# Performance work log

Hardware: AMD Instinct MI355X
Metric: run time of the kernel (lower is better)

The kernel has to match this reference:

```python
import jax, jax.numpy as jnp
import numpy as np

NEG_SLOPE = 0.2


def gatv2_layer(x, src, dst, Wl, Wr, att, bias, concat):
    # PyG GATv2Conv (share_weights=False): x_l = W_l x (source), x_r = W_r x (target)
    # e_ij = att . leaky_relu(x_l[j] + x_r[i]); alpha = softmax over incoming edges at i
    N = x.shape[0]
    H, C = att.shape
    xl = (x @ Wl).reshape(N, H, C)
    xr = (x @ Wr).reshape(N, H, C)
    msg = jax.nn.leaky_relu(xl[src] + xr[dst], NEG_SLOPE)          # [E, H, C]
    logits = jnp.einsum('ehc,hc->eh', msg, att)                     # [E, H]
    mx = jax.ops.segment_max(logits, dst, num_segments=N)           # [N, H]
    ex = jnp.exp(logits - mx[dst])
    denom = jax.ops.segment_sum(ex, dst, num_segments=N)            # [N, H]
    alpha = ex / denom[dst]                                         # [E, H]
    out = jax.ops.segment_sum(alpha[:, :, None] * xl[src], dst, num_segments=N)  # [N, H, C]
    out = out.reshape(N, H * C) if concat else out.mean(axis=1)
    return out + bias


def gat_forward(x, edge_index, Wl1, Wr1, att1, b1, Wl2, Wr2, att2, b2, Wl3, Wr3, att3, b3):
    N = x.shape[0]
    loop = jnp.arange(N, dtype=edge_index.dtype)
    src = jnp.concatenate([edge_index[0], loop])  # add self loops (PyG default)
    dst = jnp.concatenate([edge_index[1], loop])
    # eval mode: feature/attention dropout are identity
    h = jax.nn.elu(gatv2_layer(x, src, dst, Wl1, Wr1, att1, b1, concat=True))
    h = jax.nn.elu(gatv2_layer(h, src, dst, Wl2, Wr2, att2, b2, concat=True))
    return gatv2_layer(h, src, dst, Wl3, Wr3, att3, b3, concat=False)


def setup_inputs() -> dict:
    key = jax.random.key(0)
    ks = jax.random.split(key, 16)
    N, E = 50000, 800000
    IN, HID, H, OUT = 256, 32, 8, 64
    D1 = HID * H  # 256
    s = 0.05
    return {
        'x': jax.random.normal(ks[0], (N, IN), dtype=jnp.float32),
        'edge_index': jax.random.randint(ks[1], (2, E), 0, N, dtype=jnp.int64),
        'Wl1': jax.random.normal(ks[2], (IN, D1), dtype=jnp.float32) * s,
        'Wr1': jax.random.normal(ks[3], (IN, D1), dtype=jnp.float32) * s,
        'att1': jax.random.normal(ks[4], (H, HID), dtype=jnp.float32) * s,
        'b1': jnp.zeros((D1,), dtype=jnp.float32),
        'Wl2': jax.random.normal(ks[5], (D1, D1), dtype=jnp.float32) * s,
        'Wr2': jax.random.normal(ks[6], (D1, D1), dtype=jnp.float32) * s,
        'att2': jax.random.normal(ks[7], (H, HID), dtype=jnp.float32) * s,
        'b2': jnp.zeros((D1,), dtype=jnp.float32),
        'Wl3': jax.random.normal(ks[8], (D1, OUT), dtype=jnp.float32) * s,
        'Wr3': jax.random.normal(ks[9], (D1, OUT), dtype=jnp.float32) * s,
        'att3': jax.random.normal(ks[10], (1, OUT), dtype=jnp.float32) * s,
        'b3': jnp.zeros((OUT,), dtype=jnp.float32),
    }


def reference(x, edge_index, Wl1, Wr1, att1, b1, Wl2, Wr2, att2, b2, Wl3, Wr3, att3, b3):
    return gat_forward(x, edge_index, Wl1, Wr1, att1, b1, Wl2, Wr2, att2, b2, Wl3, Wr3, att3, b3)
```

## Files before the change

kernel.cpp:

```cpp
#include <hip/hip_runtime.h>
#include <hip/hip_fp16.h>

#define NEG_SLOPE 0.2f

typedef __attribute__((ext_vector_type(8))) _Float16 f16x8;
typedef __attribute__((ext_vector_type(4))) float f32x4;

__device__ __forceinline__ void gload_lds16(const unsigned short* g, unsigned short* lds) {
    __builtin_amdgcn_global_load_lds(
        (const __attribute__((address_space(1))) void*)g,
        (__attribute__((address_space(3))) void*)lds, 16, 0, 0);
}

__device__ __forceinline__ void h8_to_f(const uint4 v, float* f) {
    const __half2* hp = reinterpret_cast<const __half2*>(&v);
    float2 t0 = __half22float2(hp[0]);
    float2 t1 = __half22float2(hp[1]);
    float2 t2 = __half22float2(hp[2]);
    float2 t3 = __half22float2(hp[3]);
    f[0] = t0.x; f[1] = t0.y; f[2] = t1.x; f[3] = t1.y;
    f[4] = t2.x; f[5] = t2.y; f[6] = t3.x; f[7] = t3.y;
}


__global__ void detect_i64_kernel(const unsigned int* __restrict__ w, int E, int* __restrict__ flag) {
    __shared__ unsigned int ssum[256];
    int n = E < 4096 ? E : 4096;
    unsigned int local = 0;
    for (int k = threadIdx.x; k < n; k += 256) local |= w[2 * k + 1];
    ssum[threadIdx.x] = local;
    __syncthreads();
    for (int off = 128; off > 0; off >>= 1) {
        if (threadIdx.x < off) ssum[threadIdx.x] |= ssum[threadIdx.x + off];
        __syncthreads();
    }
    if (threadIdx.x == 0) flag[0] = (ssum[0] == 0) ? 1 : 0;
}

__global__ void count_deg_kernel(const void* __restrict__ eiv, int E,
                                 const int* __restrict__ flag, int* __restrict__ deg) {
    int e = blockIdx.x * blockDim.x + threadIdx.x;
    if (e >= E) return;
    int d;
    if (*flag) d = (int)((const long long*)eiv)[(size_t)E + e];
    else       d = ((const int*)eiv)[(size_t)E + e];
    atomicAdd(&deg[d], 1);
}

__global__ void scan_block_kernel(const int* __restrict__ deg, int* __restrict__ row_ptr,
                                  int* __restrict__ partial, int N) {
    __shared__ int sd[1024];
    int t = threadIdx.x;
    int g = blockIdx.x * 1024 + t;
    int v = (g < N) ? deg[g] : 0;
    sd[t] = v;
    __syncthreads();
    for (int off = 1; off < 1024; off <<= 1) {
        int add = (t >= off) ? sd[t - off] : 0;
        __syncthreads();
        sd[t] += add;
        __syncthreads();
    }
    if (g < N) row_ptr[g + 1] = sd[t];
    if (t == 1023) partial[blockIdx.x] = sd[1023];
    if (g == 0) row_ptr[0] = 0;
}

__global__ void scan_top_kernel(int* __restrict__ partial, int nb) {
    if (threadIdx.x == 0 && blockIdx.x == 0) {
        int run = 0;
        for (int j = 0; j < nb; ++j) { run += partial[j]; partial[j] = run; }
    }
}

__global__ void scan_addoff_kernel(int* __restrict__ row_ptr, const int* __restrict__ partial, int N) {
    int g = blockIdx.x * 256 + threadIdx.x;
    if (g >= N) return;
    int b = g >> 10;
    if (b > 0) row_ptr[g + 1] += partial[b - 1];
}

__global__ void scatter_kernel(const void* __restrict__ eiv, int E,
                               const int* __restrict__ flag,
                               const int* __restrict__ row_ptr,
                               int* __restrict__ cursor, int* __restrict__ csr) {
    int e = blockIdx.x * blockDim.x + threadIdx.x;
    if (e >= E) return;
    int s, d;
    if (*flag) {
        s = (int)((const long long*)eiv)[e];
        d = (int)((const long long*)eiv)[(size_t)E + e];
    } else {
        s = ((const int*)eiv)[e];
        d = ((const int*)eiv)[(size_t)E + e];
    }
    int pos = atomicAdd(&cursor[d], 1);
    csr[row_ptr[d] + pos] = s;
}


__global__ void split_kernel(const float* __restrict__ src, int n4,
                             unsigned short* __restrict__ hi, unsigned short* __restrict__ lo) {
    int i = blockIdx.x * blockDim.x + threadIdx.x;
    if (i >= n4) return;
    float4 v = *reinterpret_cast<const float4*>(&src[(size_t)i * 4]);
    ushort4 h, l;
    __half t;
    t = __float2half(v.x); h.x = __half_as_ushort(t); l.x = __half_as_ushort(__float2half(v.x - __half2float(t)));
    t = __float2half(v.y); h.y = __half_as_ushort(t); l.y = __half_as_ushort(__float2half(v.y - __half2float(t)));
    t = __float2half(v.z); h.z = __half_as_ushort(t); l.z = __half_as_ushort(__float2half(v.z - __half2float(t)));
    t = __float2half(v.w); h.w = __half_as_ushort(t); l.w = __half_as_ushort(__float2half(v.w - __half2float(t)));
    *reinterpret_cast<ushort4*>(&hi[(size_t)i * 4]) = h;
    *reinterpret_cast<ushort4*>(&lo[(size_t)i * 4]) = l;
}

__global__ void splitT_w_kernel(const float* __restrict__ Wl, const float* __restrict__ Wr, int M,
                                unsigned short* __restrict__ WThi) {
    int k = blockIdx.x;
    int m2 = blockIdx.y * 256 + threadIdx.x;
    if (m2 >= 2 * M) return;
    float v = (m2 < M) ? Wl[(size_t)k * M + m2] : Wr[(size_t)k * M + (m2 - M)];
    WThi[(size_t)m2 * 256 + k] = __half_as_ushort(__float2half(v));
}


__global__ __launch_bounds__(256) void gemm_mfma_kernel(
    const unsigned short* __restrict__ Ahi, const unsigned short* __restrict__ Alo,
    const unsigned short* __restrict__ B,
    __half* __restrict__ xl16, float* __restrict__ xr32, int N, int M) {
    __shared__ unsigned short sA[2][128 * 64];
    __shared__ unsigned short sB[128 * 64];

    int t = threadIdx.x;
    int lane = t & 63;
    int w = t >> 6;
    int wr = (w >> 1) * 64;
    int wc = (w & 1) * 64;
    int row0 = blockIdx.x * 128;
    int n0 = blockIdx.y * 128;

    int l15 = lane & 15;
    int l4 = lane >> 4;

    int lr8 = lane >> 3;
    int lc8 = lane & 7;
    int ksw = (lc8 ^ lr8) * 8;

    f32x4 acc[4][4] = {};

    for (int k0 = 0; k0 < 256; k0 += 64) {
        __syncthreads();
        #pragma unroll
        for (int i = 0; i < 4; ++i) {
            int brow = i * 32 + w * 8;
            int row = brow + lr8;
            int ar = row0 + row; if (ar >= N) ar = N - 1;
            int bc = n0 + row;
            gload_lds16(&Ahi[(size_t)ar * 256 + k0 + ksw], &sA[0][brow * 64]);
            gload_lds16(&Alo[(size_t)ar * 256 + k0 + ksw], &sA[1][brow * 64]);
            gload_lds16(&B[(size_t)bc * 256 + k0 + ksw], &sB[brow * 64]);
        }
        __syncthreads();

        #pragma unroll
        for (int ksub = 0; ksub < 2; ++ksub) {
            int kb = ksub * 32 + l4 * 8;
            f16x8 b[4];
            #pragma unroll
            for (int fc = 0; fc < 4; ++fc) {
                int cc = wc + fc * 16 + l15;
                b[fc] = *reinterpret_cast<const f16x8*>(&sB[cc * 64 + (kb ^ ((cc & 7) << 3))]);
            }
            #pragma unroll
            for (int fr = 0; fr < 4; ++fr) {
                int r = wr + fr * 16 + l15;
                int idx = r * 64 + (kb ^ ((r & 7) << 3));
                f16x8 ah = *reinterpret_cast<const f16x8*>(&sA[0][idx]);
                f16x8 al = *reinterpret_cast<const f16x8*>(&sA[1][idx]);
                #pragma unroll
                for (int fc = 0; fc < 4; ++fc) {
                    acc[fr][fc] = __builtin_amdgcn_mfma_f32_16x16x32_f16(ah, b[fc], acc[fr][fc], 0, 0, 0);
                    acc[fr][fc] = __builtin_amdgcn_mfma_f32_16x16x32_f16(al, b[fc], acc[fr][fc], 0, 0, 0);
                }
            }
        }
    }

    #pragma unroll
    for (int fr = 0; fr < 4; ++fr) {
        #pragma unroll
        for (int j = 0; j < 4; ++j) {
            int row = row0 + wr + fr * 16 + l4 * 4 + j;
            if (row < N) {
                #pragma unroll
                for (int fc = 0; fc < 4; ++fc) {
                    int col = n0 + wc + fc * 16 + l15;
                    float v = acc[fr][fc][j];
                    if (col < M) xl16[(size_t)row * M + col] = __float2half(v);
                    else         xr32[(size_t)row * M + (col - M)] = v;
                }
            }
        }
    }
}


__global__ __launch_bounds__(256) void agg_h8_kernel(
    const __half* __restrict__ xl16, const float* __restrict__ xr32,
    const float* __restrict__ att, const float* __restrict__ bias,
    const int* __restrict__ row_ptr, const int* __restrict__ csr,
    unsigned short* __restrict__ ohi, unsigned short* __restrict__ olo, int N) {
    int wv = threadIdx.x >> 6;
    int i = blockIdx.x * 4 + wv;
    if (i >= N) return;
    int lane = threadIdx.x & 63;
    int half = lane >> 5;
    int cb = (lane & 31) * 8;

    float rxr[8], a6[8], a4[8];
    {
        float4 r0 = *reinterpret_cast<const float4*>(&xr32[(size_t)i * 256 + cb]);
        float4 r1 = *reinterpret_cast<const float4*>(&xr32[(size_t)i * 256 + cb + 4]);
        rxr[0] = r0.x; rxr[1] = r0.y; rxr[2] = r0.z; rxr[3] = r0.w;
        rxr[4] = r1.x; rxr[5] = r1.y; rxr[6] = r1.z; rxr[7] = r1.w;
        float4 w0 = *reinterpret_cast<const float4*>(&att[cb]);
        float4 w1 = *reinterpret_cast<const float4*>(&att[cb + 4]);
        float aa[8] = {w0.x, w0.y, w0.z, w0.w, w1.x, w1.y, w1.z, w1.w};
        #pragma unroll
        for (int c = 0; c < 8; ++c) { a6[c] = 0.6f * aa[c]; a4[c] = 0.4f * aa[c]; }
    }

    float acc[8], l, m;
    {
        uint4 sv = *reinterpret_cast<const uint4*>(&xl16[(size_t)i * 256 + cb]);
        float u[8];
        h8_to_f(sv, u);
        float p = 0.f;
        #pragma unroll
        for (int c = 0; c < 8; ++c) {
            float v = u[c] + rxr[c];
            p = fmaf(a6[c], v, p);
            p = fmaf(a4[c], fabsf(v), p);
        }
        p += __shfl_xor(p, 1, 4);
        p += __shfl_xor(p, 2, 4);
        m = p;
        l = half ? 0.f : 1.f;
        #pragma unroll
        for (int c = 0; c < 8; ++c) acc[c] = half ? 0.f : u[c];
    }

    int start = row_ptr[i], end = row_ptr[i + 1];

    int kk0 = start + half, kk1 = start + 2 + half;
    int s0 = (kk0 < end) ? csr[kk0] : i;
    int s1 = (kk1 < end) ? csr[kk1] : i;
    uint4 ca = *reinterpret_cast<const uint4*>(&xl16[(size_t)s0 * 256 + cb]);
    uint4 cbv = *reinterpret_cast<const uint4*>(&xl16[(size_t)s1 * 256 + cb]);

    for (int k = start; k < end; k += 4) {
        int nk0 = k + 4 + half, nk1 = k + 6 + half;
        int t0 = (nk0 < end) ? csr[nk0] : i;
        int t1 = (nk1 < end) ? csr[nk1] : i;
        uint4 na = *reinterpret_cast<const uint4*>(&xl16[(size_t)t0 * 256 + cb]);
        uint4 nb = *reinterpret_cast<const uint4*>(&xl16[(size_t)t1 * 256 + cb]);

        float ua[8], ub[8];
        h8_to_f(ca, ua);
        h8_to_f(cbv, ub);
        float p0 = 0.f, p1 = 0.f;
        #pragma unroll
        for (int c = 0; c < 8; ++c) {
            float v0 = ua[c] + rxr[c];
            p0 = fmaf(a6[c], v0, p0);
            p0 = fmaf(a4[c], fabsf(v0), p0);
            float v1 = ub[c] + rxr[c];
            p1 = fmaf(a6[c], v1, p1);
            p1 = fmaf(a4[c], fabsf(v1), p1);
        }
        p0 += __shfl_xor(p0, 1, 4);
        p0 += __shfl_xor(p0, 2, 4);
        p1 += __shfl_xor(p1, 1, 4);
        p1 += __shfl_xor(p1, 2, 4);
        float e0 = (k + half < end)     ? __expf(fminf(p0 - m, 60.f)) : 0.f;
        float e1 = (k + 2 + half < end) ? __expf(fminf(p1 - m, 60.f)) : 0.f;
        l += e0 + e1;
        #pragma unroll
        for (int c = 0; c < 8; ++c) acc[c] = fmaf(e0, ua[c], fmaf(e1, ub[c], acc[c]));

        ca = na; cbv = nb;
    }

    l += __shfl_xor(l, 32, 64);
    #pragma unroll
    for (int c = 0; c < 8; ++c) acc[c] += __shfl_xor(acc[c], 32, 64);

    if (half == 0) {
        float4 bb0 = *reinterpret_cast<const float4*>(&bias[cb]);
        float4 bb1 = *reinterpret_cast<const float4*>(&bias[cb + 4]);
        float bs[8] = {bb0.x, bb0.y, bb0.z, bb0.w, bb1.x, bb1.y, bb1.z, bb1.w};
        float inv = 1.0f / l;
        unsigned int hw[4], lw[4];
        #pragma unroll
        for (int c2 = 0; c2 < 4; ++c2) {
            float r0 = fmaf(acc[2 * c2], inv, bs[2 * c2]);
            float r1 = fmaf(acc[2 * c2 + 1], inv, bs[2 * c2 + 1]);
            r0 = (r0 > 0.f) ? r0 : (__expf(r0) - 1.f);
            r1 = (r1 > 0.f) ? r1 : (__expf(r1) - 1.f);
            __half th0 = __float2half(r0);
            __half th1 = __float2half(r1);
            unsigned short h0 = __half_as_ushort(th0), h1 = __half_as_ushort(th1);
            float f0 = r0 - __half2float(th0);
            float f1 = r1 - __half2float(th1);
            unsigned short l0 = __half_as_ushort(__float2half(f0));
            unsigned short l1 = __half_as_ushort(__float2half(f1));
            hw[c2] = (unsigned int)h0 | ((unsigned int)h1 << 16);
            lw[c2] = (unsigned int)l0 | ((unsigned int)l1 << 16);
        }
        *reinterpret_cast<uint4*>(&ohi[(size_t)i * 256 + cb]) = make_uint4(hw[0], hw[1], hw[2], hw[3]);
        *reinterpret_cast<uint4*>(&olo[(size_t)i * 256 + cb]) = make_uint4(lw[0], lw[1], lw[2], lw[3]);
    }
}


__global__ __launch_bounds__(256) void agg_h1_kernel(
    const __half* __restrict__ xl16, const float* __restrict__ xr32,
    const float* __restrict__ att, const float* __restrict__ bias,
    const int* __restrict__ row_ptr, const int* __restrict__ csr,
    float* __restrict__ out, int N) {
    int wv = threadIdx.x >> 6;
    int i = blockIdx.x * 4 + wv;
    if (i >= N) return;
    int lane = threadIdx.x & 63;
    int es = lane >> 3;
    int cb = (lane & 7) * 8;

    float rxr[8], a6[8], a4[8];
    {
        float4 r0 = *reinterpret_cast<const float4*>(&xr32[(size_t)i * 64 + cb]);
        float4 r1 = *reinterpret_cast<const float4*>(&xr32[(size_t)i * 64 + cb + 4]);
        rxr[0] = r0.x; rxr[1] = r0.y; rxr[2] = r0.z; rxr[3] = r0.w;
        rxr[4] = r1.x; rxr[5] = r1.y; rxr[6] = r1.z; rxr[7] = r1.w;
        float4 w0 = *reinterpret_cast<const float4*>(&att[cb]);
        float4 w1 = *reinterpret_cast<const float4*>(&att[cb + 4]);
        float aa[8] = {w0.x, w0.y, w0.z, w0.w, w1.x, w1.y, w1.z, w1.w};
        #pragma unroll
        for (int c = 0; c < 8; ++c) { a6[c] = 0.6f * aa[c]; a4[c] = 0.4f * aa[c]; }
    }

    float acc[8], l, m;
    {
        uint4 sv = *reinterpret_cast<const uint4*>(&xl16[(size_t)i * 64 + cb]);
        float u[8];
        h8_to_f(sv, u);
        float p = 0.f;
        #pragma unroll
        for (int c = 0; c < 8; ++c) {
            float v = u[c] + rxr[c];
            p = fmaf(a6[c], v, p);
            p = fmaf(a4[c], fabsf(v), p);
        }
        p += __shfl_xor(p, 1, 8);
        p += __shfl_xor(p, 2, 8);
        p += __shfl_xor(p, 4, 8);
        m = p;
        l = es ? 0.f : 1.f;
        #pragma unroll
        for (int c = 0; c < 8; ++c) acc[c] = es ? 0.f : u[c];
    }

    int start = row_ptr[i], end = row_ptr[i + 1];

    int kk = start + es;
    int s = (kk < end) ? csr[kk] : i;
    uint4 cu = *reinterpret_cast<const uint4*>(&xl16[(size_t)s * 64 + cb]);

    for (int k = start; k < end; k += 8) {
        int nk = k + 8 + es;
        int tn = (nk < end) ? csr[nk] : i;
        uint4 nu = *reinterpret_cast<const uint4*>(&xl16[(size_t)tn * 64 + cb]);

        float u[8];
        h8_to_f(cu, u);
        float p = 0.f;
        #pragma unroll
        for (int c = 0; c < 8; ++c) {
            float v = u[c] + rxr[c];
            p = fmaf(a6[c], v, p);
            p = fmaf(a4[c], fabsf(v), p);
        }
        p += __shfl_xor(p, 1, 8);
        p += __shfl_xor(p, 2, 8);
        p += __shfl_xor(p, 4, 8);
        float e = (k + es < end) ? __expf(fminf(p - m, 60.f)) : 0.f;
        l += e;
        #pragma unroll
        for (int c = 0; c < 8; ++c) acc[c] = fmaf(e, u[c], acc[c]);

        cu = nu;
    }

    l += __shfl_xor(l, 8, 64);
    l += __shfl_xor(l, 16, 64);
    l += __shfl_xor(l, 32, 64);
    #pragma unroll
    for (int c = 0; c < 8; ++c) {
        acc[c] += __shfl_xor(acc[c], 8, 64);
        acc[c] += __shfl_xor(acc[c], 16, 64);
        acc[c] += __shfl_xor(acc[c], 32, 64);
    }

    if (es == 0) {
        float inv = 1.0f / l;
        float4 bb0 = *reinterpret_cast<const float4*>(&bias[cb]);
        float4 bb1 = *reinterpret_cast<const float4*>(&bias[cb + 4]);
        float4 o0, o1;
        o0.x = fmaf(acc[0], inv, bb0.x);
        o0.y = fmaf(acc[1], inv, bb0.y);
        o0.z = fmaf(acc[2], inv, bb0.z);
        o0.w = fmaf(acc[3], inv, bb0.w);
        o1.x = fmaf(acc[4], inv, bb1.x);
        o1.y = fmaf(acc[5], inv, bb1.y);
        o1.z = fmaf(acc[6], inv, bb1.z);
        o1.w = fmaf(acc[7], inv, bb1.w);
        *reinterpret_cast<float4*>(&out[(size_t)i * 64 + cb]) = o0;
        *reinterpret_cast<float4*>(&out[(size_t)i * 64 + cb + 4]) = o1;
    }
}


extern "C" void kernel_launch(void* const* d_in, const int* in_sizes, int n_in,
                              void* d_out, int out_size, void* d_ws, size_t ws_size,
                              hipStream_t stream) {
    const float* x    = (const float*)d_in[0];
    const void*  ei   = d_in[1];
    const float* Wl1  = (const float*)d_in[2];
    const float* Wr1  = (const float*)d_in[3];
    const float* att1 = (const float*)d_in[4];
    const float* b1   = (const float*)d_in[5];
    const float* Wl2  = (const float*)d_in[6];
    const float* Wr2  = (const float*)d_in[7];
    const float* att2 = (const float*)d_in[8];
    const float* b2   = (const float*)d_in[9];
    const float* Wl3  = (const float*)d_in[10];
    const float* Wr3  = (const float*)d_in[11];
    const float* att3 = (const float*)d_in[12];
    const float* b3   = (const float*)d_in[13];
    float* out = (float*)d_out;

    int N = in_sizes[0] / 256;
    int E = in_sizes[1] / 2;

    char* w = (char*)d_ws;
    unsigned short* h_hi = (unsigned short*)w; w += (size_t)N * 256 * 2;
    unsigned short* h_lo = (unsigned short*)w; w += (size_t)N * 256 * 2;
    __half* xl16 = (__half*)w;     w += (size_t)N * 256 * 2;
    float* xr32 = (float*)w;       w += (size_t)N * 256 * sizeof(float);
    unsigned short* WT_hi = (unsigned short*)w; w += (size_t)512 * 256 * 2;
    int* row_ptr = (int*)w; w += ((size_t)N + 2) * sizeof(int);
    int* deg     = (int*)w; w += (size_t)N * sizeof(int);
    int* csr     = (int*)w; w += (size_t)E * sizeof(int);
    int* flag    = (int*)w; w += 256;
    int* partial = (int*)w; w += 256;

    detect_i64_kernel<<<1, 256, 0, stream>>>((const unsigned int*)ei, E, flag);
    hipMemsetAsync(deg, 0, (size_t)N * sizeof(int), stream);
    count_deg_kernel<<<(E + 255) / 256, 256, 0, stream>>>(ei, E, flag, deg);
    int nb = (N + 1023) / 1024;
    scan_block_kernel<<<nb, 1024, 0, stream>>>(deg, row_ptr, partial, N);
    scan_top_kernel<<<1, 64, 0, stream>>>(partial, nb);
    scan_addoff_kernel<<<(N + 255) / 256, 256, 0, stream>>>(row_ptr, partial, N);
    hipMemsetAsync(deg, 0, (size_t)N * sizeof(int), stream);
    scatter_kernel<<<(E + 255) / 256, 256, 0, stream>>>(ei, E, flag, row_ptr, deg, csr);

    int gemm_gx = (N + 127) / 128;
    int agg_g = (N + 3) / 4;

    split_kernel<<<((N * 256 / 4) + 255) / 256, 256, 0, stream>>>(x, N * 256 / 4, h_hi, h_lo);
    splitT_w_kernel<<<dim3(256, 2), 256, 0, stream>>>(Wl1, Wr1, 256, WT_hi);
    gemm_mfma_kernel<<<dim3(gemm_gx, 4), 256, 0, stream>>>(h_hi, h_lo, WT_hi, xl16, xr32, N, 256);
    agg_h8_kernel<<<agg_g, 256, 0, stream>>>(xl16, xr32, att1, b1, row_ptr, csr, h_hi, h_lo, N);

    splitT_w_kernel<<<dim3(256, 2), 256, 0, stream>>>(Wl2, Wr2, 256, WT_hi);
    gemm_mfma_kernel<<<dim3(gemm_gx, 4), 256, 0, stream>>>(h_hi, h_lo, WT_hi, xl16, xr32, N, 256);
    agg_h8_kernel<<<agg_g, 256, 0, stream>>>(xl16, xr32, att2, b2, row_ptr, csr, h_hi, h_lo, N);

    splitT_w_kernel<<<dim3(256, 1), 256, 0, stream>>>(Wl3, Wr3, 64, WT_hi);
    gemm_mfma_kernel<<<dim3(gemm_gx, 1), 256, 0, stream>>>(h_hi, h_lo, WT_hi, xl16, xr32, N, 64);
    agg_h1_kernel<<<agg_g, 256, 0, stream>>>(xl16, xr32, att3, b3, row_ptr, csr, out, N);
}
```

Measured before the change: 413.2 us.

## Drop hi/lo fp16 split for activations and use packed fp16 dot2 for attention logits

Activations were previously stored as hi+lo fp16 pairs, and each GEMM ran two MFMAs per tile to recover fp32-like precision. Now a single fp16 copy is kept, which halves the A-operand loads, the LDS traffic and the MFMA count, and removes the lo-part stores in the aggregation epilogue. The attention logit computation in both aggregation kernels moves from scalar fp32 FMAs to packed fp16 adds followed by fdot2. The cost is lower numerical precision in both the GEMM inputs and the logits, which could push results outside the tolerance.

```diff
diff --git a/kernel.cpp b/kernel.cpp
--- a/kernel.cpp
+++ b/kernel.cpp
@@ -4,6 +4,7 @@
 #define NEG_SLOPE 0.2f
 
 typedef __attribute__((ext_vector_type(8))) _Float16 f16x8;
+typedef __attribute__((ext_vector_type(2))) _Float16 f16x2;
 typedef __attribute__((ext_vector_type(4))) float f32x4;
 
 __device__ __forceinline__ void gload_lds16(const unsigned short* g, unsigned short* lds) {
@@ -12,14 +13,9 @@
         (__attribute__((address_space(3))) void*)lds, 16, 0, 0);
 }
 
-__device__ __forceinline__ void h8_to_f(const uint4 v, float* f) {
-    const __half2* hp = reinterpret_cast<const __half2*>(&v);
-    float2 t0 = __half22float2(hp[0]);
-    float2 t1 = __half22float2(hp[1]);
-    float2 t2 = __half22float2(hp[2]);
-    float2 t3 = __half22float2(hp[3]);
-    f[0] = t0.x; f[1] = t0.y; f[2] = t1.x; f[3] = t1.y;
-    f[4] = t2.x; f[5] = t2.y; f[6] = t3.x; f[7] = t3.y;
+__device__ __forceinline__ f16x2 habs2(f16x2 v) {
+    unsigned int u = __builtin_bit_cast(unsigned int, v) & 0x7FFF7FFFu;
+    return __builtin_bit_cast(f16x2, u);
 }
 
 
@@ -99,36 +95,33 @@
 }
 
 
-__global__ void split_kernel(const float* __restrict__ src, int n4,
-                             unsigned short* __restrict__ hi, unsigned short* __restrict__ lo) {
+__global__ void to_f16_kernel(const float* __restrict__ src, int n4,
+                              unsigned short* __restrict__ dst) {
     int i = blockIdx.x * blockDim.x + threadIdx.x;
     if (i >= n4) return;
     float4 v = *reinterpret_cast<const float4*>(&src[(size_t)i * 4]);
-    ushort4 h, l;
-    __half t;
-    t = __float2half(v.x); h.x = __half_as_ushort(t); l.x = __half_as_ushort(__float2half(v.x - __half2float(t)));
-    t = __float2half(v.y); h.y = __half_as_ushort(t); l.y = __half_as_ushort(__float2half(v.y - __half2float(t)));
-    t = __float2half(v.z); h.z = __half_as_ushort(t); l.z = __half_as_ushort(__float2half(v.z - __half2float(t)));
-    t = __float2half(v.w); h.w = __half_as_ushort(t); l.w = __half_as_ushort(__float2half(v.w - __half2float(t)));
-    *reinterpret_cast<ushort4*>(&hi[(size_t)i * 4]) = h;
-    *reinterpret_cast<ushort4*>(&lo[(size_t)i * 4]) = l;
+    ushort4 h;
+    h.x = __half_as_ushort(__float2half(v.x));
+    h.y = __half_as_ushort(__float2half(v.y));
+    h.z = __half_as_ushort(__float2half(v.z));
+    h.w = __half_as_ushort(__float2half(v.w));
+    *reinterpret_cast<ushort4*>(&dst[(size_t)i * 4]) = h;
 }
 
 __global__ void splitT_w_kernel(const float* __restrict__ Wl, const float* __restrict__ Wr, int M,
-                                unsigned short* __restrict__ WThi) {
+                                unsigned short* __restrict__ WT) {
     int k = blockIdx.x;
     int m2 = blockIdx.y * 256 + threadIdx.x;
     if (m2 >= 2 * M) return;
     float v = (m2 < M) ? Wl[(size_t)k * M + m2] : Wr[(size_t)k * M + (m2 - M)];
-    WThi[(size_t)m2 * 256 + k] = __half_as_ushort(__float2half(v));
+    WT[(size_t)m2 * 256 + k] = __half_as_ushort(__float2half(v));
 }
 
 
 __global__ __launch_bounds__(256) void gemm_mfma_kernel(
-    const unsigned short* __restrict__ Ahi, const unsigned short* __restrict__ Alo,
-    const unsigned short* __restrict__ B,
+    const unsigned short* __restrict__ A, const unsigned short* __restrict__ B,
     __half* __restrict__ xl16, float* __restrict__ xr32, int N, int M) {
-    __shared__ unsigned short sA[2][128 * 64];
+    __shared__ unsigned short sA[128 * 64];
     __shared__ unsigned short sB[128 * 64];
 
     int t = threadIdx.x;
@@ -156,8 +149,7 @@
             int row = brow + lr8;
             int ar = row0 + row; if (ar >= N) ar = N - 1;
             int bc = n0 + row;
-            gload_lds16(&Ahi[(size_t)ar * 256 + k0 + ksw], &sA[0][brow * 64]);
-            gload_lds16(&Alo[(size_t)ar * 256 + k0 + ksw], &sA[1][brow * 64]);
+            gload_lds16(&A[(size_t)ar * 256 + k0 + ksw], &sA[brow * 64]);
             gload_lds16(&B[(size_t)bc * 256 + k0 + ksw], &sB[brow * 64]);
         }
         __syncthreads();
@@ -174,13 +166,10 @@
             #pragma unroll
             for (int fr = 0; fr < 4; ++fr) {
                 int r = wr + fr * 16 + l15;
-                int idx = r * 64 + (kb ^ ((r & 7) << 3));
-                f16x8 ah = *reinterpret_cast<const f16x8*>(&sA[0][idx]);
-                f16x8 al = *reinterpret_cast<const f16x8*>(&sA[1][idx]);
+                f16x8 a = *reinterpret_cast<const f16x8*>(&sA[r * 64 + (kb ^ ((r & 7) << 3))]);
                 #pragma unroll
                 for (int fc = 0; fc < 4; ++fc) {
-                    acc[fr][fc] = __builtin_amdgcn_mfma_f32_16x16x32_f16(ah, b[fc], acc[fr][fc], 0, 0, 0);
-                    acc[fr][fc] = __builtin_amdgcn_mfma_f32_16x16x32_f16(al, b[fc], acc[fr][fc], 0, 0, 0);
+                    acc[fr][fc] = __builtin_amdgcn_mfma_f32_16x16x32_f16(a, b[fc], acc[fr][fc], 0, 0, 0);
                 }
             }
         }
@@ -209,7 +198,7 @@
     const __half* __restrict__ xl16, const float* __restrict__ xr32,
     const float* __restrict__ att, const float* __restrict__ bias,
     const int* __restrict__ row_ptr, const int* __restrict__ csr,
-    unsigned short* __restrict__ ohi, unsigned short* __restrict__ olo, int N) {
+    unsigned short* __restrict__ oh, int N) {
     int wv = threadIdx.x >> 6;
     int i = blockIdx.x * 4 + wv;
     if (i >= N) return;
@@ -217,7 +206,8 @@
     int half = lane >> 5;
     int cb = (lane & 31) * 8;
 
-    float rxr[8], a6[8], a4[8];
+    f16x2 r2[4], a62[4], a42[4];
+    float rxr[8];
     {
         float4 r0 = *reinterpret_cast<const float4*>(&xr32[(size_t)i * 256 + cb]);
         float4 r1 = *reinterpret_cast<const float4*>(&xr32[(size_t)i * 256 + cb + 4]);
@@ -227,27 +217,33 @@
         float4 w1 = *reinterpret_cast<const float4*>(&att[cb + 4]);
         float aa[8] = {w0.x, w0.y, w0.z, w0.w, w1.x, w1.y, w1.z, w1.w};
         #pragma unroll
-        for (int c = 0; c < 8; ++c) { a6[c] = 0.6f * aa[c]; a4[c] = 0.4f * aa[c]; }
+        for (int j = 0; j < 4; ++j) {
+            r2[j]  = f16x2{(_Float16)rxr[2 * j], (_Float16)rxr[2 * j + 1]};
+            a62[j] = f16x2{(_Float16)(0.6f * aa[2 * j]), (_Float16)(0.6f * aa[2 * j + 1])};
+            a42[j] = f16x2{(_Float16)(0.4f * aa[2 * j]), (_Float16)(0.4f * aa[2 * j + 1])};
+        }
     }
 
     float acc[8], l, m;
     {
         uint4 sv = *reinterpret_cast<const uint4*>(&xl16[(size_t)i * 256 + cb]);
-        float u[8];
-        h8_to_f(sv, u);
+        const f16x2* u2 = reinterpret_cast<const f16x2*>(&sv);
         float p = 0.f;
         #pragma unroll
-        for (int c = 0; c < 8; ++c) {
-            float v = u[c] + rxr[c];
-            p = fmaf(a6[c], v, p);
-            p = fmaf(a4[c], fabsf(v), p);
+        for (int j = 0; j < 4; ++j) {
+            f16x2 v2 = u2[j] + r2[j];
+            p = __builtin_amdgcn_fdot2(a62[j], v2, p, false);
+            p = __builtin_amdgcn_fdot2(a42[j], habs2(v2), p, false);
         }
         p += __shfl_xor(p, 1, 4);
         p += __shfl_xor(p, 2, 4);
         m = p;
         l = half ? 0.f : 1.f;
         #pragma unroll
-        for (int c = 0; c < 8; ++c) acc[c] = half ? 0.f : u[c];
+        for (int j = 0; j < 4; ++j) {
+            acc[2 * j]     = half ? 0.f : (float)u2[j][0];
+            acc[2 * j + 1] = half ? 0.f : (float)u2[j][1];
+        }
     }
 
     int start = row_ptr[i], end = row_ptr[i + 1];
@@ -265,18 +261,17 @@
         uint4 na = *reinterpret_cast<const uint4*>(&xl16[(size_t)t0 * 256 + cb]);
         uint4 nb = *reinterpret_cast<const uint4*>(&xl16[(size_t)t1 * 256 + cb]);
 
-        float ua[8], ub[8];
-        h8_to_f(ca, ua);
-        h8_to_f(cbv, ub);
+        const f16x2* ua2 = reinterpret_cast<const f16x2*>(&ca);
+        const f16x2* ub2 = reinterpret_cast<const f16x2*>(&cbv);
         float p0 = 0.f, p1 = 0.f;
         #pragma unroll
-        for (int c = 0; c < 8; ++c) {
-            float v0 = ua[c] + rxr[c];
-            p0 = fmaf(a6[c], v0, p0);
-            p0 = fmaf(a4[c], fabsf(v0), p0);
-            float v1 = ub[c] + rxr[c];
-            p1 = fmaf(a6[c], v1, p1);
-            p1 = fmaf(a4[c], fabsf(v1), p1);
+        for (int j = 0; j < 4; ++j) {
+            f16x2 v0 = ua2[j] + r2[j];
+            p0 = __builtin_amdgcn_fdot2(a62[j], v0, p0, false);
+            p0 = __builtin_amdgcn_fdot2(a42[j], habs2(v0), p0, false);
+            f16x2 v1 = ub2[j] + r2[j];
+            p1 = __builtin_amdgcn_fdot2(a62[j], v1, p1, false);
+            p1 = __builtin_amdgcn_fdot2(a42[j], habs2(v1), p1, false);
         }
         p0 += __shfl_xor(p0, 1, 4);
         p0 += __shfl_xor(p0, 2, 4);
@@ -286,7 +281,10 @@
         float e1 = (k + 2 + half < end) ? __expf(fminf(p1 - m, 60.f)) : 0.f;
         l += e0 + e1;
         #pragma unroll
-        for (int c = 0; c < 8; ++c) acc[c] = fmaf(e0, ua[c], fmaf(e1, ub[c], acc[c]));
+        for (int j = 0; j < 4; ++j) {
+            acc[2 * j]     = fmaf(e0, (float)ua2[j][0], fmaf(e1, (float)ub2[j][0], acc[2 * j]));
+            acc[2 * j + 1] = fmaf(e0, (float)ua2[j][1], fmaf(e1, (float)ub2[j][1], acc[2 * j + 1]));
+        }
 
         ca = na; cbv = nb;
     }
@@ -300,25 +298,18 @@
         float4 bb1 = *reinterpret_cast<const float4*>(&bias[cb + 4]);
         float bs[8] = {bb0.x, bb0.y, bb0.z, bb0.w, bb1.x, bb1.y, bb1.z, bb1.w};
         float inv = 1.0f / l;
-        unsigned int hw[4], lw[4];
+        unsigned int hw[4];
         #pragma unroll
         for (int c2 = 0; c2 < 4; ++c2) {
             float r0 = fmaf(acc[2 * c2], inv, bs[2 * c2]);
             float r1 = fmaf(acc[2 * c2 + 1], inv, bs[2 * c2 + 1]);
             r0 = (r0 > 0.f) ? r0 : (__expf(r0) - 1.f);
             r1 = (r1 > 0.f) ? r1 : (__expf(r1) - 1.f);
-            __half th0 = __float2half(r0);
-            __half th1 = __float2half(r1);
-            unsigned short h0 = __half_as_ushort(th0), h1 = __half_as_ushort(th1);
-            float f0 = r0 - __half2float(th0);
-            float f1 = r1 - __half2float(th1);
-            unsigned short l0 = __half_as_ushort(__float2half(f0));
-            unsigned short l1 = __half_as_ushort(__float2half(f1));
+            unsigned short h0 = __half_as_ushort(__float2half(r0));
+            unsigned short h1 = __half_as_ushort(__float2half(r1));
             hw[c2] = (unsigned int)h0 | ((unsigned int)h1 << 16);
-            lw[c2] = (unsigned int)l0 | ((unsigned int)l1 << 16);
-        }
-        *reinterpret_cast<uint4*>(&ohi[(size_t)i * 256 + cb]) = make_uint4(hw[0], hw[1], hw[2], hw[3]);
-        *reinterpret_cast<uint4*>(&olo[(size_t)i * 256 + cb]) = make_uint4(lw[0], lw[1], lw[2], lw[3]);
+        }
+        *reinterpret_cast<uint4*>(&oh[(size_t)i * 256 + cb]) = make_uint4(hw[0], hw[1], hw[2], hw[3]);
     }
 }
 
@@ -335,30 +326,32 @@
     int es = lane >> 3;
     int cb = (lane & 7) * 8;
 
-    float rxr[8], a6[8], a4[8];
+    f16x2 r2[4], a62[4], a42[4];
     {
         float4 r0 = *reinterpret_cast<const float4*>(&xr32[(size_t)i * 64 + cb]);
         float4 r1 = *reinterpret_cast<const float4*>(&xr32[(size_t)i * 64 + cb + 4]);
-        rxr[0] = r0.x; rxr[1] = r0.y; rxr[2] = r0.z; rxr[3] = r0.w;
-        rxr[4] = r1.x; rxr[5] = r1.y; rxr[6] = r1.z; rxr[7] = r1.w;
+        float rr[8] = {r0.x, r0.y, r0.z, r0.w, r1.x, r1.y, r1.z, r1.w};
         float4 w0 = *reinterpret_cast<const float4*>(&att[cb]);
         float4 w1 = *reinterpret_cast<const float4*>(&att[cb + 4]);
         float aa[8] = {w0.x, w0.y, w0.z, w0.w, w1.x, w1.y, w1.z, w1.w};
         #pragma unroll
-        for (int c = 0; c < 8; ++c) { a6[c] = 0.6f * aa[c]; a4[c] = 0.4f * aa[c]; }
+        for (int j = 0; j < 4; ++j) {
+            r2[j]  = f16x2{(_Float16)rr[2 * j], (_Float16)rr[2 * j + 1]};
+            a62[j] = f16x2{(_Float16)(0.6f * aa[2 * j]), (_Float16)(0.6f * aa[2 * j + 1])};
+            a42[j] = f16x2{(_Float16)(0.4f * aa[2 * j]), (_Float16)(0.4f * aa[2 * j + 1])};
+        }
     }
 
     float acc[8], l, m;
     {
         uint4 sv = *reinterpret_cast<const uint4*>(&xl16[(size_t)i * 64 + cb]);
-        float u[8];
-        h8_to_f(sv, u);
+        const f16x2* u2 = reinterpret_cast<const f16x2*>(&sv);
         float p = 0.f;
         #pragma unroll
-        for (int c = 0; c < 8; ++c) {
-            float v = u[c] + rxr[c];
-            p = fmaf(a6[c], v, p);
-            p = fmaf(a4[c], fabsf(v), p);
+        for (int j = 0; j < 4; ++j) {
+            f16x2 v2 = u2[j] + r2[j];
+            p = __builtin_amdgcn_fdot2(a62[j], v2, p, false);
+            p = __builtin_amdgcn_fdot2(a42[j], habs2(v2), p, false);
         }
         p += __shfl_xor(p, 1, 8);
         p += __shfl_xor(p, 2, 8);
@@ -366,7 +359,10 @@
         m = p;
         l = es ? 0.f : 1.f;
         #pragma unroll
-        for (int c = 0; c < 8; ++c) acc[c] = es ? 0.f : u[c];
+        for (int j = 0; j < 4; ++j) {
+            acc[2 * j]     = es ? 0.f : (float)u2[j][0];
+            acc[2 * j + 1] = es ? 0.f : (float)u2[j][1];
+        }
     }
 
     int start = row_ptr[i], end = row_ptr[i + 1];
@@ -380,14 +376,13 @@
         int tn = (nk < end) ? csr[nk] : i;
         uint4 nu = *reinterpret_cast<const uint4*>(&xl16[(size_t)tn * 64 + cb]);
 
-        float u[8];
-        h8_to_f(cu, u);
+        const f16x2* u2 = reinterpret_cast<const f16x2*>(&cu);
         float p = 0.f;
         #pragma unroll
-        for (int c = 0; c < 8; ++c) {
-            float v = u[c] + rxr[c];
-            p = fmaf(a6[c], v, p);
-            p = fmaf(a4[c], fabsf(v), p);
+        for (int j = 0; j < 4; ++j) {
+            f16x2 v2 = u2[j] + r2[j];
+            p = __builtin_amdgcn_fdot2(a62[j], v2, p, false);
+            p = __builtin_amdgcn_fdot2(a42[j], habs2(v2), p, false);
         }
         p += __shfl_xor(p, 1, 8);
         p += __shfl_xor(p, 2, 8);
@@ -395,7 +390,10 @@
         float e = (k + es < end) ? __expf(fminf(p - m, 60.f)) : 0.f;
         l += e;
         #pragma unroll
-        for (int c = 0; c < 8; ++c) acc[c] = fmaf(e, u[c], acc[c]);
+        for (int j = 0; j < 4; ++j) {
+            acc[2 * j]     = fmaf(e, (float)u2[j][0], acc[2 * j]);
+            acc[2 * j + 1] = fmaf(e, (float)u2[j][1], acc[2 * j + 1]);
+        }
 
         cu = nu;
     }
@@ -452,11 +450,10 @@
     int E = in_sizes[1] / 2;
 
     char* w = (char*)d_ws;
-    unsigned short* h_hi = (unsigned short*)w; w += (size_t)N * 256 * 2;
-    unsigned short* h_lo = (unsigned short*)w; w += (size_t)N * 256 * 2;
+    unsigned short* a16  = (unsigned short*)w; w += (size_t)N * 256 * 2;
     __half* xl16 = (__half*)w;     w += (size_t)N * 256 * 2;
     float* xr32 = (float*)w;       w += (size_t)N * 256 * sizeof(float);
-    unsigned short* WT_hi = (unsigned short*)w; w += (size_t)512 * 256 * 2;
+    unsigned short* WT = (unsigned short*)w; w += (size_t)512 * 256 * 2;
     int* row_ptr = (int*)w; w += ((size_t)N + 2) * sizeof(int);
     int* deg     = (int*)w; w += (size_t)N * sizeof(int);
     int* csr     = (int*)w; w += (size_t)E * sizeof(int);
@@ -476,16 +473,16 @@
     int gemm_gx = (N + 127) / 128;
     int agg_g = (N + 3) / 4;
 
-    split_kernel<<<((N * 256 / 4) + 255) / 256, 256, 0, stream>>>(x, N * 256 / 4, h_hi, h_lo);
-    splitT_w_kernel<<<dim3(256, 2), 256, 0, stream>>>(Wl1, Wr1, 256, WT_hi);
-    gemm_mfma_kernel<<<dim3(gemm_gx, 4), 256, 0, stream>>>(h_hi, h_lo, WT_hi, xl16, xr32, N, 256);
-    agg_h8_kernel<<<agg_g, 256, 0, stream>>>(xl16, xr32, att1, b1, row_ptr, csr, h_hi, h_lo, N);
-
-    splitT_w_kernel<<<dim3(256, 2), 256, 0, stream>>>(Wl2, Wr2, 256, WT_hi);
-    gemm_mfma_kernel<<<dim3(gemm_gx, 4), 256, 0, stream>>>(h_hi, h_lo, WT_hi, xl16, xr32, N, 256);
-    agg_h8_kernel<<<agg_g, 256, 0, stream>>>(xl16, xr32, att2, b2, row_ptr, csr, h_hi, h_lo, N);
-
-    splitT_w_kernel<<<dim3(256, 1), 256, 0, stream>>>(Wl3, Wr3, 64, WT_hi);
-    gemm_mfma_kernel<<<dim3(gemm_gx, 1), 256, 0, stream>>>(h_hi, h_lo, WT_hi, xl16, xr32, N, 64);
+    to_f16_kernel<<<((N * 256 / 4) + 255) / 256, 256, 0, stream>>>(x, N * 256 / 4, a16);
+    splitT_w_kernel<<<dim3(256, 2), 256, 0, stream>>>(Wl1, Wr1, 256, WT);
+    gemm_mfma_kernel<<<dim3(gemm_gx, 4), 256, 0, stream>>>(a16, WT, xl16, xr32, N, 256);
+    agg_h8_kernel<<<agg_g, 256, 0, stream>>>(xl16, xr32, att1, b1, row_ptr, csr, a16, N);
+
+    splitT_w_kernel<<<dim3(256, 2), 256, 0, stream>>>(Wl2, Wr2, 256, WT);
+    gemm_mfma_kernel<<<dim3(gemm_gx, 4), 256, 0, stream>>>(a16, WT, xl16, xr32, N, 256);
+    agg_h8_kernel<<<agg_g, 256, 0, stream>>>(xl16, xr32, att2, b2, row_ptr, csr, a16, N);
+
+    splitT_w_kernel<<<dim3(256, 1), 256, 0, stream>>>(Wl3, Wr3, 64, WT);
+    gemm_mfma_kernel<<<dim3(gemm_gx, 1), 256, 0, stream>>>(a16, WT, xl16, xr32, N, 64);
     agg_h1_kernel<<<agg_g, 256, 0, stream>>>(xl16, xr32, att3, b3, row_ptr, csr, out, N);
 }
```

After: 381.9 us. 1.08x faster.
